# Performance work log

Measured on AMD Instinct MI355X. Metric: run time of the kernel, lower is better.

The kernel has to match this reference:

```python
import jax, jax.numpy as jnp
import numpy as np

B, S, K, N = 4, 2048, 4096, 11008  # batch, seq, in_features, out_features

def setup_inputs() -> dict:
    key = jax.random.key(0)
    k1, k2, k3, k4 = jax.random.split(key, 4)
    x = jax.random.normal(k1, (B, S, K), dtype=jnp.float32)
    weight = jax.random.normal(k2, (N, K), dtype=jnp.float32) * 0.02
    # per-output-channel dequant scales, positive
    wscales = jax.random.uniform(k3, (N, 1), dtype=jnp.float32, minval=0.5, maxval=1.5)
    bias = jax.random.normal(k4, (1, N), dtype=jnp.float32) * 0.01
    return {"x": x, "weight": weight, "wscales": wscales, "bias": bias}

def reference(x, weight, wscales, bias):
    # Faithful to UniCoreLinearFP4.forward:
    #   weight_dequant = weight * wscales   (per-out-channel scale)
    #   out = x_2d @ weight_dequant.T, reshape, + bias
    x2 = x.reshape(-1, weight.shape[1])          # [B*S, K]
    w_dequant = weight * wscales                  # [N, K]
    out = x2 @ w_dequant.T                        # [B*S, N]
    out = out.reshape(*x.shape[:-1], weight.shape[0])
    out = out + bias
    return out
```

## Files before the change

kernel.cpp:

```cpp
#include <hip/hip_runtime.h>
#include <cstdint>
#include <cstddef>

#define K_DIM 4096
#define BM 256
#define BN 256
#define BK 32
#define NTILES (K_DIM / BK)

typedef __bf16 bf16x8 __attribute__((ext_vector_type(8)));
typedef float  f32x4  __attribute__((ext_vector_type(4)));
typedef unsigned int u32x4 __attribute__((ext_vector_type(4)));

__device__ __forceinline__ unsigned int pack2_bf16_rne(float lo, float hi) {
    unsigned int ulo = __float_as_uint(lo);
    unsigned int uhi = __float_as_uint(hi);
    ulo += 0x7fffu + ((ulo >> 16) & 1u);
    uhi += 0x7fffu + ((uhi >> 16) & 1u);
    return (ulo >> 16) | (uhi & 0xffff0000u);
}

__global__ void cvt_x_kernel(const float* __restrict__ in,
                             unsigned short* __restrict__ out, size_t n8) {
    size_t i = (size_t)blockIdx.x * blockDim.x + threadIdx.x;
    if (i >= n8) return;
    const f32x4* p = (const f32x4*)in + i * 2;
    f32x4 a = __builtin_nontemporal_load(p);
    f32x4 b = __builtin_nontemporal_load(p + 1);
    u32x4 r;
    r.x = pack2_bf16_rne(a.x, a.y);
    r.y = pack2_bf16_rne(a.z, a.w);
    r.z = pack2_bf16_rne(b.x, b.y);
    r.w = pack2_bf16_rne(b.z, b.w);
    *((u32x4*)out + i) = r;
}

__global__ void cvt_w_kernel(const float* __restrict__ w,
                             const float* __restrict__ s,
                             unsigned short* __restrict__ out, size_t n8) {
    size_t i = (size_t)blockIdx.x * blockDim.x + threadIdx.x;
    if (i >= n8) return;
    int row = (int)((i * 8) >> 12);
    float sc = s[row];
    const f32x4* p = (const f32x4*)w + i * 2;
    f32x4 a = __builtin_nontemporal_load(p);
    f32x4 b = __builtin_nontemporal_load(p + 1);
    u32x4 r;
    r.x = pack2_bf16_rne(a.x * sc, a.y * sc);
    r.y = pack2_bf16_rne(a.z * sc, a.w * sc);
    r.z = pack2_bf16_rne(b.x * sc, b.y * sc);
    r.w = pack2_bf16_rne(b.z * sc, b.w * sc);
    *((u32x4*)out + i) = r;
}

__global__ __launch_bounds__(512, 2)
void gemm_bf16_256(const unsigned short* __restrict__ A,
                   const unsigned short* __restrict__ B,
                   const float* __restrict__ bias,
                   float* __restrict__ C, int M, int N) {
    __shared__ __attribute__((aligned(16))) unsigned short lds[4 * 16384];

    const int t  = threadIdx.x;
    const int l  = t & 63;
    const int w  = t >> 6;
    const int wm = w >> 2;
    const int wn = w & 3;

    const int num_m = M / BM;
    const int num_n = N / BN;
    const int nwg   = num_m * num_n;

    int bid = blockIdx.x;
    int nq = nwg >> 3, nr = nwg & 7;
    int xcd = bid & 7, off = bid >> 3;
    int swz = (xcd < nr ? xcd * (nq + 1) : nr * (nq + 1) + (xcd - nr) * nq) + off;

    const int GM = 4;
    int wide = GM * num_n;
    int gid = swz / wide;
    int first_m = gid * GM;
    int gsz = min(GM, num_m - first_m);
    int pm = first_m + (swz % gsz);
    int pn = (swz % wide) / gsz;
    const int rowBase = pm * BM;
    const int colBase = pn * BN;

    const int sRow = t >> 2;
    const int gck  = (t & 3) ^ ((t >> 3) & 3);
    const unsigned short* gA0 = A + (size_t)(rowBase + sRow) * K_DIM + gck * 8;
    const unsigned short* gB0 = B + (size_t)(colBase + sRow) * K_DIM + gck * 8;

    const int q  = l >> 4;
    const int mn = l & 15;
    const int qp = q ^ ((mn >> 1) & 3);
    const int aBase =        (wm * 128 + mn) * BK + qp * 8;
    const int bBase = 8192 + (wn *  64 + mn) * BK + qp * 8;

#define GLDS(gp, lo)                                                          \
    __builtin_amdgcn_global_load_lds(                                         \
        (const __attribute__((address_space(1))) unsigned int*)(gp),          \
        (__attribute__((address_space(3))) unsigned int*)(&lds[lo]), 16, 0, 0)

#define STAGE_A(tt) do { const int _bo = ((tt) & 3) * 16384;                  \
    GLDS(gA0 + (size_t)(tt) * BK,                        _bo +         t * 8);\
    GLDS(gA0 + (size_t)(tt) * BK + (size_t)128 * K_DIM,  _bo + 4096  + t * 8);\
    } while (0)
#define STAGE_B(tt) do { const int _bo = ((tt) & 3) * 16384;                  \
    GLDS(gB0 + (size_t)(tt) * BK,                        _bo + 8192  + t * 8);\
    GLDS(gB0 + (size_t)(tt) * BK + (size_t)128 * K_DIM,  _bo + 12288 + t * 8);\
    } while (0)

    f32x4 acc[8][4];
#pragma unroll
    for (int i = 0; i < 8; i++)
#pragma unroll
        for (int j = 0; j < 4; j++) acc[i][j] = (f32x4){0.f, 0.f, 0.f, 0.f};

    STAGE_A(0); STAGE_B(0);
    STAGE_A(1); STAGE_B(1);
    STAGE_A(2); STAGE_B(2);
    asm volatile("s_waitcnt vmcnt(8)" ::: "memory");
    __builtin_amdgcn_s_barrier();

    for (int tt = 0; tt < NTILES; ++tt) {
        const int bo = (tt & 3) * 16384;
        bf16x8 aF[4], bF[4];

#pragma unroll
        for (int j = 0; j < 4; j++) bF[j] = *(const bf16x8*)&lds[bo + bBase + j * 512];
#pragma unroll
        for (int i = 0; i < 4; i++) aF[i] = *(const bf16x8*)&lds[bo + aBase + i * 512];
        if (tt + 3 < NTILES) STAGE_A(tt + 3);
        __builtin_amdgcn_s_barrier();
        asm volatile("s_waitcnt lgkmcnt(0)" ::: "memory");
        __builtin_amdgcn_sched_barrier(0);
        __builtin_amdgcn_s_setprio(1);
#pragma unroll
        for (int i = 0; i < 4; i++)
#pragma unroll
            for (int j = 0; j < 4; j++)
                acc[i][j] = __builtin_amdgcn_mfma_f32_16x16x32_bf16(aF[i], bF[j], acc[i][j], 0, 0, 0);
        __builtin_amdgcn_s_setprio(0);
        __builtin_amdgcn_s_barrier();

#pragma unroll
        for (int i = 0; i < 4; i++) aF[i] = *(const bf16x8*)&lds[bo + aBase + (i + 4) * 512];
        if (tt + 3 < NTILES) STAGE_B(tt + 3);
        __builtin_amdgcn_s_barrier();
        asm volatile("s_waitcnt lgkmcnt(0)" ::: "memory");
        __builtin_amdgcn_sched_barrier(0);
        __builtin_amdgcn_s_setprio(1);
#pragma unroll
        for (int i = 0; i < 4; i++)
#pragma unroll
            for (int j = 0; j < 4; j++)
                acc[i + 4][j] = __builtin_amdgcn_mfma_f32_16x16x32_bf16(aF[i], bF[j], acc[i + 4][j], 0, 0, 0);
        __builtin_amdgcn_s_setprio(0);

        if (tt + 3 < NTILES)      asm volatile("s_waitcnt vmcnt(8)" ::: "memory");
        else if (tt + 2 < NTILES) asm volatile("s_waitcnt vmcnt(4)" ::: "memory");
        else if (tt + 1 < NTILES) asm volatile("s_waitcnt vmcnt(0)" ::: "memory");
        __builtin_amdgcn_s_barrier();
    }

#undef GLDS
#undef STAGE_A
#undef STAGE_B

#pragma unroll
    for (int j = 0; j < 4; j++) {
        const int col = colBase + wn * 64 + j * 16 + mn;
        const float bv = bias[col];
#pragma unroll
        for (int i = 0; i < 8; i++) {
            const int row0 = rowBase + wm * 128 + i * 16 + q * 4;
#pragma unroll
            for (int r = 0; r < 4; r++) {
                __builtin_nontemporal_store(acc[i][j][r] + bv,
                                            &C[(size_t)(row0 + r) * N + col]);
            }
        }
    }
}

__global__ void gemm_f32_fallback(const float* __restrict__ X,
                                  const float* __restrict__ W,
                                  const float* __restrict__ S,
                                  const float* __restrict__ bias,
                                  float* __restrict__ C, int M, int N) {
    __shared__ float sx[16][17];
    __shared__ float sw[16][17];
    int tx = threadIdx.x, ty = threadIdx.y;
    int row = blockIdx.y * 16 + ty;
    int col = blockIdx.x * 16 + tx;
    float acc = 0.f;
    for (int k0 = 0; k0 < K_DIM; k0 += 16) {
        sx[ty][tx] = X[(size_t)row * K_DIM + k0 + tx];
        sw[ty][tx] = W[(size_t)(blockIdx.x * 16 + ty) * K_DIM + k0 + tx];
        __syncthreads();
#pragma unroll
        for (int kk = 0; kk < 16; kk++) acc += sx[ty][kk] * sw[tx][kk];
        __syncthreads();
    }
    C[(size_t)row * N + col] = acc * S[col] + bias[col];
}

extern "C" void kernel_launch(void* const* d_in, const int* in_sizes, int n_in,
                              void* d_out, int out_size, void* d_ws, size_t ws_size,
                              hipStream_t stream) {
    const float* x    = (const float*)d_in[0];
    const float* wgt  = (const float*)d_in[1];
    const float* wsc  = (const float*)d_in[2];
    const float* bias = (const float*)d_in[3];
    float* out = (float*)d_out;

    const size_t M = (size_t)in_sizes[0] / K_DIM;
    const size_t N = (size_t)in_sizes[2];

    const size_t xb_elems = M * K_DIM;
    const size_t wb_elems = N * K_DIM;
    const size_t need = (xb_elems + wb_elems) * sizeof(unsigned short);

    if (ws_size >= need && (M % BM) == 0 && (N % BN) == 0) {
        unsigned short* xb = (unsigned short*)d_ws;
        unsigned short* wb = xb + xb_elems;
        cvt_x_kernel<<<dim3((unsigned)(xb_elems / 8 / 256)), 256, 0, stream>>>(x, xb, xb_elems / 8);
        cvt_w_kernel<<<dim3((unsigned)(wb_elems / 8 / 256)), 256, 0, stream>>>(wgt, wsc, wb, wb_elems / 8);
        const unsigned nblk = (unsigned)((M / BM) * (N / BN));
        gemm_bf16_256<<<dim3(nblk), 512, 0, stream>>>(xb, wb, bias, out, (int)M, (int)N);
    } else {
        gemm_f32_fallback<<<dim3((unsigned)(N / 16), (unsigned)(M / 16)), dim3(16, 16), 0, stream>>>(
            x, wgt, wsc, bias, out, (int)M, (int)N);
    }
}
```

Before: 1.189 ms.

## Software-pipeline LDS fragment loads across MFMA phases with double-buffered B registers

Restructures the main GEMM loop so that LDS reads for the next half-tile and the next K-tile are issued before the MFMA block that consumes the current fragments, using partial lgkmcnt waits instead of full drains. The B fragments are ping-ponged between two register sets by unrolling the loop by two, and the first-tile fragments are preloaded before the loop. This is meant to hide LDS latency behind matrix-core work and drop one barrier per phase, at the cost of more live VGPRs and tighter reliance on correct waitcnt and barrier ordering.

```diff
diff --git a/kernel.cpp b/kernel.cpp
--- a/kernel.cpp
+++ b/kernel.cpp
@@ -116,53 +116,73 @@
 #pragma unroll
         for (int j = 0; j < 4; j++) acc[i][j] = (f32x4){0.f, 0.f, 0.f, 0.f};
 
+    bf16x8 aCur[4], aMid[4], bP[4], bQ[4];
+
     STAGE_A(0); STAGE_B(0);
     STAGE_A(1); STAGE_B(1);
     STAGE_A(2); STAGE_B(2);
     asm volatile("s_waitcnt vmcnt(8)" ::: "memory");
     __builtin_amdgcn_s_barrier();
-
-    for (int tt = 0; tt < NTILES; ++tt) {
-        const int bo = (tt & 3) * 16384;
-        bf16x8 aF[4], bF[4];
-
-#pragma unroll
-        for (int j = 0; j < 4; j++) bF[j] = *(const bf16x8*)&lds[bo + bBase + j * 512];
-#pragma unroll
-        for (int i = 0; i < 4; i++) aF[i] = *(const bf16x8*)&lds[bo + aBase + i * 512];
-        if (tt + 3 < NTILES) STAGE_A(tt + 3);
-        __builtin_amdgcn_s_barrier();
-        asm volatile("s_waitcnt lgkmcnt(0)" ::: "memory");
-        __builtin_amdgcn_sched_barrier(0);
-        __builtin_amdgcn_s_setprio(1);
-#pragma unroll
-        for (int i = 0; i < 4; i++)
-#pragma unroll
-            for (int j = 0; j < 4; j++)
-                acc[i][j] = __builtin_amdgcn_mfma_f32_16x16x32_bf16(aF[i], bF[j], acc[i][j], 0, 0, 0);
-        __builtin_amdgcn_s_setprio(0);
-        __builtin_amdgcn_s_barrier();
-
-#pragma unroll
-        for (int i = 0; i < 4; i++) aF[i] = *(const bf16x8*)&lds[bo + aBase + (i + 4) * 512];
-        if (tt + 3 < NTILES) STAGE_B(tt + 3);
-        __builtin_amdgcn_s_barrier();
-        asm volatile("s_waitcnt lgkmcnt(0)" ::: "memory");
-        __builtin_amdgcn_sched_barrier(0);
-        __builtin_amdgcn_s_setprio(1);
-#pragma unroll
-        for (int i = 0; i < 4; i++)
-#pragma unroll
-            for (int j = 0; j < 4; j++)
-                acc[i + 4][j] = __builtin_amdgcn_mfma_f32_16x16x32_bf16(aF[i], bF[j], acc[i + 4][j], 0, 0, 0);
-        __builtin_amdgcn_s_setprio(0);
-
-        if (tt + 3 < NTILES)      asm volatile("s_waitcnt vmcnt(8)" ::: "memory");
-        else if (tt + 2 < NTILES) asm volatile("s_waitcnt vmcnt(4)" ::: "memory");
-        else if (tt + 1 < NTILES) asm volatile("s_waitcnt vmcnt(0)" ::: "memory");
-        __builtin_amdgcn_s_barrier();
-    }
-
+#pragma unroll
+    for (int i = 0; i < 4; i++) aCur[i] = *(const bf16x8*)&lds[aBase + i * 512];
+#pragma unroll
+    for (int j = 0; j < 4; j++) bP[j]   = *(const bf16x8*)&lds[bBase + j * 512];
+
+#define TILE_BODY(tt, bCur, bNxt)                                             \
+    {                                                                         \
+        const int bo  = ((tt) & 3) * 16384;                                   \
+        const int bo1 = (((tt) + 1) & 3) * 16384;                             \
+        _Pragma("unroll")                                                     \
+        for (int i = 0; i < 4; i++)                                           \
+            aMid[i] = *(const bf16x8*)&lds[bo + aBase + (i + 4) * 512];       \
+        if ((tt) + 3 < NTILES) STAGE_A((tt) + 3);                             \
+        asm volatile("s_waitcnt lgkmcnt(4)" ::: "memory");                    \
+        __builtin_amdgcn_sched_barrier(0);                                    \
+        __builtin_amdgcn_s_setprio(1);                                        \
+        _Pragma("unroll")                                                     \
+        for (int i = 0; i < 4; i++)                                           \
+            _Pragma("unroll")                                                 \
+            for (int j = 0; j < 4; j++)                                       \
+                acc[i][j] = __builtin_amdgcn_mfma_f32_16x16x32_bf16(          \
+                    aCur[i], bCur[j], acc[i][j], 0, 0, 0);                    \
+        __builtin_amdgcn_s_setprio(0);                                        \
+        if ((tt) <= NTILES - 4)                                               \
+            asm volatile("s_waitcnt vmcnt(6)" ::: "memory");                  \
+        else if ((tt) == NTILES - 3)                                          \
+            asm volatile("s_waitcnt vmcnt(4)" ::: "memory");                  \
+        else                                                                  \
+            asm volatile("s_waitcnt vmcnt(0)" ::: "memory");                  \
+        __builtin_amdgcn_s_barrier();     \
+        if ((tt) + 1 < NTILES) {                                              \
+            _Pragma("unroll")                                                 \
+            for (int i = 0; i < 4; i++)                                       \
+                aCur[i] = *(const bf16x8*)&lds[bo1 + aBase + i * 512];        \
+            _Pragma("unroll")                                                 \
+            for (int j = 0; j < 4; j++)                                       \
+                bNxt[j] = *(const bf16x8*)&lds[bo1 + bBase + j * 512];        \
+            if ((tt) + 3 < NTILES) STAGE_B((tt) + 3);                         \
+            asm volatile("s_waitcnt lgkmcnt(8)" ::: "memory");                \
+        } else {                                                              \
+            asm volatile("s_waitcnt lgkmcnt(0)" ::: "memory");                \
+        }                                                                     \
+        __builtin_amdgcn_sched_barrier(0);                                    \
+        __builtin_amdgcn_s_setprio(1);                                        \
+        _Pragma("unroll")                                                     \
+        for (int i = 0; i < 4; i++)                                           \
+            _Pragma("unroll")                                                 \
+            for (int j = 0; j < 4; j++)                                       \
+                acc[i + 4][j] = __builtin_amdgcn_mfma_f32_16x16x32_bf16(      \
+                    aMid[i], bCur[j], acc[i + 4][j], 0, 0, 0);                \
+        __builtin_amdgcn_s_setprio(0);                                        \
+        __builtin_amdgcn_s_barrier();         \
+    }
+
+    for (int tt = 0; tt < NTILES; tt += 2) {
+        TILE_BODY(tt,     bP, bQ);
+        TILE_BODY(tt + 1, bQ, bP);
+    }
+
+#undef TILE_BODY
 #undef GLDS
 #undef STAGE_A
 #undef STAGE_B
```

New measurement: 1.148 ms. -3.5%, faster.
